# Performance work log

Measured on AMD Instinct MI355X. Metric: run time of the kernel, lower is better.

Reference implementation:

```python
import jax, jax.numpy as jnp
import numpy as np

EPS = 1e-5


def _cbr(z, W, bn, relu=True):
    # z: [b, Cin, L]; W: [Cout, Cin]; bn: [4, Cout] = (gamma, beta, mean, var)
    # 1x1 Conv2d (bias=False) over a [b, Cin, L, 1] tensor == channel matmul.
    y = jnp.einsum('oi,bil->bol', W, z)
    g, b_, m, v = bn[0], bn[1], bn[2], bn[3]
    y = g[:, None] * (y - m[:, None]) * jax.lax.rsqrt(v[:, None] + EPS) + b_[:, None]
    return jax.nn.relu(y) if relu else y


def setup_inputs() -> dict:
    key = jax.random.key(0)
    ks = jax.random.split(key, 13)
    b, c, h, w = 32, 512, 48, 48
    in_spatial = h * w          # 2304
    inter_spatial = in_spatial // 4  # 576
    inter_channel = c // 4      # 128
    ncc = 1 + inter_channel     # 129
    return {
        'x': jax.random.normal(ks[0], (b, c, h, w), jnp.float32),
        'W_theta': jax.random.normal(ks[1], (inter_spatial, in_spatial), jnp.float32) * 0.02,
        'bn_theta': jax.random.uniform(ks[2], (4, inter_spatial), jnp.float32),
        'W_phi': jax.random.normal(ks[3], (inter_spatial, in_spatial), jnp.float32) * 0.02,
        'bn_phi': jax.random.uniform(ks[4], (4, inter_spatial), jnp.float32),
        'W_gx': jax.random.normal(ks[5], (inter_spatial, in_spatial), jnp.float32) * 0.02,
        'bn_gx': jax.random.uniform(ks[6], (4, inter_spatial), jnp.float32),
        'W_gg': jax.random.normal(ks[7], (inter_channel, 2 * c), jnp.float32) * 0.02,
        'bn_gg': jax.random.uniform(ks[8], (4, inter_channel), jnp.float32),
        'W_c1': jax.random.normal(ks[9], (ncc // 2, ncc), jnp.float32) * 0.02,
        'bn_c1': jax.random.uniform(ks[10], (4, ncc // 2), jnp.float32),
        'W_c2': jax.random.normal(ks[11], (1, ncc // 2), jnp.float32) * 0.02,
        'bn_c2': jax.random.uniform(ks[12], (4, 1), jnp.float32),
    }


def reference(x, W_theta, bn_theta, W_phi, bn_phi, W_gx, bn_gx,
              W_gg, bn_gg, W_c1, bn_c1, W_c2, bn_c2):
    b, c, h, w = x.shape
    xc = x.reshape(b, c, h * w).transpose(0, 2, 1)          # [b, hw, c]
    xc1 = _cbr(xc, W_theta, bn_theta).transpose(0, 2, 1)    # [b, c, is]
    xc2 = _cbr(xc, W_phi, bn_phi)                           # [b, is, c]
    Gc = jnp.einsum('bcs,bsd->bcd', xc1, xc2)               # [b, c, c]
    Gc_joint = jnp.concatenate([Gc.transpose(0, 2, 1), Gc], axis=1)  # [b, 2c, c]
    Gc_joint = _cbr(Gc_joint, W_gg, bn_gg)                  # [b, ic, c]
    g_xc = _cbr(xc, W_gx, bn_gx).mean(axis=1, keepdims=True)  # [b, 1, c]
    yc = jnp.concatenate([g_xc, Gc_joint], axis=1)          # [b, 1+ic, c]
    wy = _cbr(yc, W_c1, bn_c1)
    wy = _cbr(wy, W_c2, bn_c2, relu=False)                  # [b, 1, c]
    gate = jax.nn.sigmoid(wy)[:, 0, :, None, None]          # [b, c, 1, 1]
    return gate * x + x
```

## Files before the change

### kernel.cpp

```cpp
#include <hip/hip_runtime.h>
#include <cstdint>

#define EPSV 1e-5f
typedef unsigned short u16;
typedef __attribute__((ext_vector_type(8))) short bh8;
typedef __attribute__((ext_vector_type(4))) float f4;

__device__ __forceinline__ float bf2f(u16 h) { return __uint_as_float((unsigned)h << 16); }
__device__ __forceinline__ u16 f2bf(float x) {
    unsigned u = __float_as_uint(x);
    u += 0x7fffu + ((u >> 16) & 1u);
    return (u16)(u >> 16);
}

__device__ __forceinline__ void gl16(const void* g, const void* s) {
    __builtin_amdgcn_global_load_lds(
        reinterpret_cast<const __attribute__((address_space(1))) void*>((uintptr_t)g),
        reinterpret_cast<__attribute__((address_space(3))) void*>((unsigned)(uintptr_t)s),
        16, 0, 0);
}

__device__ __forceinline__ void core2(
    const u16* __restrict__ Ah, const u16* __restrict__ Al,
    const u16* __restrict__ Bh, const u16* __restrict__ Bl,
    long ldA, long ldB, int K, int rowA0, int rowB0,
    u16* lds, f4 acc[4][4])
{
    const int tid = threadIdx.x, l = tid & 63, w = tid >> 6;
    const int wr = w >> 1, wc = w & 1;
    const int srow = tid >> 2;
    const int schunk = ((tid & 3) ^ ((tid >> 3) & 3)) << 3;
    const size_t aoff = (size_t)(rowA0 + srow) * ldA + schunk;
    const size_t boff = (size_t)(rowB0 + srow) * ldB + schunk;
    const size_t a64 = (size_t)64 * ldA, b64 = (size_t)64 * ldB;
    const int rr = l & 15, cq = l >> 4;
    const int roff = rr * 64 + (((cq ^ ((rr >> 1) & 3))) << 4);
    char* const base0 = (char*)lds;
    char* const base1 = (char*)lds + 32768;
    const int nt = K >> 5;

#define STAGE_SWZ(base, s0) do { \
    gl16(Ah + aoff + (s0),       (base) +         w * 1024); \
    gl16(Ah + aoff + a64 + (s0), (base) +  4096 + w * 1024); \
    gl16(Al + aoff + (s0),       (base) +  8192 + w * 1024); \
    gl16(Al + aoff + a64 + (s0), (base) + 12288 + w * 1024); \
    gl16(Bh + boff + (s0),       (base) + 16384 + w * 1024); \
    gl16(Bh + boff + b64 + (s0), (base) + 20480 + w * 1024); \
    gl16(Bl + boff + (s0),       (base) + 24576 + w * 1024); \
    gl16(Bl + boff + b64 + (s0), (base) + 28672 + w * 1024); \
} while (0)

    STAGE_SWZ(base0, 0);
    __syncthreads();
    int p = 0;
    for (int t = 0; t < nt; ++t) {
        if (t + 1 < nt) STAGE_SWZ(p ? base0 : base1, (size_t)(t + 1) << 5);
        const char* buf = p ? base1 : base0;
        bh8 a_h[4], a_l[4], b_h[4], b_l[4];
#pragma unroll
        for (int i = 0; i < 4; ++i) {
            a_h[i] = *(const bh8*)(buf + (wr * 4 + i) * 1024 + roff);
            a_l[i] = *(const bh8*)(buf + 8192 + (wr * 4 + i) * 1024 + roff);
            b_h[i] = *(const bh8*)(buf + 16384 + (wc * 4 + i) * 1024 + roff);
            b_l[i] = *(const bh8*)(buf + 24576 + (wc * 4 + i) * 1024 + roff);
        }
#pragma unroll
        for (int i = 0; i < 4; ++i)
#pragma unroll
            for (int j = 0; j < 4; ++j)
                acc[i][j] = __builtin_amdgcn_mfma_f32_16x16x32_bf16(a_h[i], b_h[j], acc[i][j], 0, 0, 0);
#pragma unroll
        for (int i = 0; i < 4; ++i)
#pragma unroll
            for (int j = 0; j < 4; ++j)
                acc[i][j] = __builtin_amdgcn_mfma_f32_16x16x32_bf16(a_h[i], b_l[j], acc[i][j], 0, 0, 0);
#pragma unroll
        for (int i = 0; i < 4; ++i)
#pragma unroll
            for (int j = 0; j < 4; ++j)
                acc[i][j] = __builtin_amdgcn_mfma_f32_16x16x32_bf16(a_l[i], b_h[j], acc[i][j], 0, 0, 0);
        __syncthreads();
        p ^= 1;
    }
#undef STAGE_SWZ
}

__global__ __launch_bounds__(256) void gemm_s1_v3(
    const u16* __restrict__ Xh, const u16* __restrict__ Xl,
    const u16* __restrict__ W0h, const u16* __restrict__ W0l,
    const u16* __restrict__ W1h, const u16* __restrict__ W1l,
    const u16* __restrict__ W2h, const u16* __restrict__ W2l,
    const float* __restrict__ bn0, const float* __restrict__ bn1,
    const float* __restrict__ bn2,
    u16* __restrict__ Y0h, u16* __restrict__ Y0l,
    u16* __restrict__ Y1h, u16* __restrict__ Y1l,
    u16* __restrict__ Y2h, u16* __restrict__ Y2l)
{
    const int h = blockIdx.x;
    const int orig = (h & 7) * 240 + (h >> 3);
    const int ow = orig % 15;
    const int rest = orig / 15;
    const int ct = rest & 3, bz = rest >> 2;
    const int wi = ow / 5, otw = ow % 5;

    const u16* Bh = wi == 0 ? W0h : wi == 1 ? W1h : W2h;
    const u16* Bl = wi == 0 ? W0l : wi == 1 ? W1l : W2l;
    const float* bnp = wi == 0 ? bn0 : wi == 1 ? bn1 : bn2;
    u16* Yh = wi == 0 ? Y0h : wi == 1 ? Y1h : Y2h;
    u16* Yl = wi == 0 ? Y0l : wi == 1 ? Y1l : Y2l;

    __shared__ u16 lds[32768];
    f4 acc[4][4];
    const f4 z4 = {0.f, 0.f, 0.f, 0.f};
#pragma unroll
    for (int i = 0; i < 4; ++i)
#pragma unroll
        for (int j = 0; j < 4; ++j) acc[i][j] = z4;

    core2(Xh, Xl, Bh, Bl, 2304, 2304, 2304,
          bz * 512 + ct * 128, otw * 128, lds, acc);

    const int l = threadIdx.x & 63, w = threadIdx.x >> 6;
    const int wr = w >> 1, wc = w & 1;
    const int mb = ct * 128 + wr * 64;
    const int nbw = otw * 128 + wc * 64;
    const int lm = l & 15;
#pragma unroll
    for (int j = 0; j < 4; ++j) {
        const int o = nbw + j * 16 + lm;
        const bool val = (o < 576);
        float sc = 0.f, sh = 0.f;
        if (val) {
            const float gg = bnp[o], be = bnp[576 + o], mm = bnp[1152 + o], vv = bnp[1728 + o];
            sc = gg * rsqrtf(vv + EPSV);
            sh = be - mm * sc;
        }
#pragma unroll
        for (int i = 0; i < 4; ++i) {
            const int c = mb + i * 16 + ((l >> 4) << 2);
#pragma unroll
            for (int r = 0; r < 4; ++r) {
                const float y = val ? fmaxf(acc[i][j][r] * sc + sh, 0.f) : 0.f;
                const u16 hh = f2bf(y);
                const u16 lo = f2bf(y - bf2f(hh));
                const size_t off = ((size_t)bz * 512 + c + r) * 640 + o;
                Yh[off] = hh; Yl[off] = lo;
            }
        }
    }
}

__global__ __launch_bounds__(256) void gemm_u(
    const u16* __restrict__ Wggh, const u16* __restrict__ Wggl,
    const u16* __restrict__ tnth, const u16* __restrict__ tntl,
    const u16* __restrict__ pnth, const u16* __restrict__ pntl,
    u16* __restrict__ U1h, u16* __restrict__ U1l,
    u16* __restrict__ U2h, u16* __restrict__ U2l)
{
    const int h = blockIdx.x;
    const int orig = (h & 7) * 40 + (h >> 3);
    const int ot = orig % 5;
    const int rest = orig / 5;
    const int u = rest & 1, b = rest >> 1;

    const u16* Ah = Wggh + (u ? 512 : 0);
    const u16* Al = Wggl + (u ? 512 : 0);
    const u16* Bh = u ? tnth : pnth;
    const u16* Bl = u ? tntl : pntl;

    __shared__ u16 lds[32768];
    f4 acc[4][4];
    const f4 z4 = {0.f, 0.f, 0.f, 0.f};
#pragma unroll
    for (int i = 0; i < 4; ++i)
#pragma unroll
        for (int j = 0; j < 4; ++j) acc[i][j] = z4;

    core2(Ah, Al, Bh, Bl, 1024, 512, 512, 0, b * 640 + ot * 128, lds, acc);

    u16* Uh = u ? U2h : U1h;
    u16* Ul = u ? U2l : U1l;
    const int l = threadIdx.x & 63, w = threadIdx.x >> 6;
    const int wr = w >> 1, wc = w & 1;
#pragma unroll
    for (int i = 0; i < 4; ++i)
#pragma unroll
        for (int j = 0; j < 4; ++j)
#pragma unroll
            for (int r = 0; r < 4; ++r) {
                const int irow = wr * 64 + i * 16 + ((l >> 4) << 2) + r;
                const int ocol = ot * 128 + wc * 64 + j * 16 + (l & 15);
                const float v = acc[i][j][r];
                const u16 hh = f2bf(v);
                const u16 lo = f2bf(v - bf2f(hh));
                const size_t off = ((size_t)b * 128 + irow) * 640 + ocol;
                Uh[off] = hh; Ul[off] = lo;
            }
}

__global__ __launch_bounds__(256) void gemm_term_p(
    const u16* __restrict__ U1h, const u16* __restrict__ U1l,
    const u16* __restrict__ U2h, const u16* __restrict__ U2l,
    const u16* __restrict__ tth, const u16* __restrict__ ttl,
    const u16* __restrict__ pth, const u16* __restrict__ ptl,
    float* __restrict__ GGa, float* __restrict__ GGb)
{
    const int h = blockIdx.x;
    const int orig = (h & 7) * 32 + (h >> 3);
    const int dt = orig & 3;
    const int u = (orig >> 2) & 1;
    const int b = orig >> 3;

    const u16* Ah = u ? U2h : U1h;
    const u16* Al = u ? U2l : U1l;
    const u16* Bh = u ? pth : tth;
    const u16* Bl = u ? ptl : ttl;
    float* G = u ? GGb : GGa;

    __shared__ u16 lds[32768];
    f4 acc[4][4];
    const f4 z4 = {0.f, 0.f, 0.f, 0.f};
#pragma unroll
    for (int i = 0; i < 4; ++i)
#pragma unroll
        for (int j = 0; j < 4; ++j) acc[i][j] = z4;

    core2(Ah, Al, Bh, Bl, 640, 640, 640,
          b * 128, b * 512 + dt * 128, lds, acc);

    const int l = threadIdx.x & 63, w = threadIdx.x >> 6;
    const int wr = w >> 1, wc = w & 1;
#pragma unroll
    for (int i = 0; i < 4; ++i)
#pragma unroll
        for (int j = 0; j < 4; ++j)
#pragma unroll
            for (int r = 0; r < 4; ++r) {
                const int irow = wr * 64 + i * 16 + ((l >> 4) << 2) + r;
                const int dcol = dt * 128 + wc * 64 + j * 16 + (l & 15);
                G[((size_t)b * 128 + irow) * 512 + dcol] = acc[i][j][r];
            }
}

__global__ __launch_bounds__(256) void gg_combine(
    float* __restrict__ GGa, const float* __restrict__ GGb,
    const float* __restrict__ bn, long n4)
{
    const long i = (long)blockIdx.x * 256 + threadIdx.x;
    if (i >= n4) return;
    const int irow = (int)((i >> 7) & 127);
    const float g = bn[irow], be = bn[128 + irow], m = bn[256 + irow], v = bn[384 + irow];
    const float sc = g * rsqrtf(v + EPSV);
    const float sh = be - m * sc;
    float4 a = ((const float4*)GGa)[i];
    const float4 b = ((const float4*)GGb)[i];
    a.x = fmaxf((a.x + b.x) * sc + sh, 0.f);
    a.y = fmaxf((a.y + b.y) * sc + sh, 0.f);
    a.z = fmaxf((a.z + b.z) * sc + sh, 0.f);
    a.w = fmaxf((a.w + b.w) * sc + sh, 0.f);
    ((float4*)GGa)[i] = a;
}

__global__ __launch_bounds__(256) void transpose_y(
    const u16* __restrict__ s0, u16* __restrict__ d0,
    const u16* __restrict__ s1, u16* __restrict__ d1,
    const u16* __restrict__ s2, u16* __restrict__ d2,
    const u16* __restrict__ s3, u16* __restrict__ d3)
{
    const int pz = blockIdx.z;
    const int b = pz >> 2, pl = pz & 3;
    const u16* src = pl == 0 ? s0 : pl == 1 ? s1 : pl == 2 ? s2 : s3;
    u16* dst = pl == 0 ? d0 : pl == 1 ? d1 : pl == 2 ? d2 : d3;
    const int o0 = blockIdx.x * 64, c0 = blockIdx.y * 64;
    __shared__ u16 t[64][72];
    const int tid = threadIdx.x;
#pragma unroll
    for (int rdx = tid; rdx < 512; rdx += 256) {
        const int c = rdx >> 3, oc = (rdx & 7) << 3;
        *(bh8*)&t[c][oc] = *(const bh8*)&src[((size_t)b * 512 + c0 + c) * 640 + o0 + oc];
    }
    __syncthreads();
#pragma unroll
    for (int wdx = tid; wdx < 512; wdx += 256) {
        const int o = wdx >> 3, cc = (wdx & 7) << 3;
        u16 v[8];
#pragma unroll
        for (int e = 0; e < 8; ++e) v[e] = t[cc + e][o];
        *(bh8*)&dst[((size_t)b * 640 + o0 + o) * 512 + c0 + cc] = *(bh8*)&v[0];
    }
}

__global__ __launch_bounds__(256) void conv_split(
    const float* __restrict__ in, u16* __restrict__ hi, u16* __restrict__ lo, long n8)
{
    long i = (long)blockIdx.x * 256 + threadIdx.x;
    const long stride = (long)gridDim.x * 256;
    for (; i < n8; i += stride) {
        const float4 a = ((const float4*)in)[2 * i];
        const float4 b = ((const float4*)in)[2 * i + 1];
        const float v[8] = {a.x, a.y, a.z, a.w, b.x, b.y, b.z, b.w};
        unsigned hw[4], lw[4];
#pragma unroll
        for (int k = 0; k < 4; ++k) {
            const u16 h0 = f2bf(v[2 * k]), h1 = f2bf(v[2 * k + 1]);
            const u16 l0 = f2bf(v[2 * k] - bf2f(h0)), l1 = f2bf(v[2 * k + 1] - bf2f(h1));
            hw[k] = (unsigned)h0 | ((unsigned)h1 << 16);
            lw[k] = (unsigned)l0 | ((unsigned)l1 << 16);
        }
        *(uint4*)&hi[8 * i] = make_uint4(hw[0], hw[1], hw[2], hw[3]);
        *(uint4*)&lo[8 * i] = make_uint4(lw[0], lw[1], lw[2], lw[3]);
    }
}

__global__ __launch_bounds__(256) void conv_w_pad(
    const float* __restrict__ W, u16* __restrict__ hi, u16* __restrict__ lo,
    int rows, long n8)
{
    const long i = (long)blockIdx.x * 256 + threadIdx.x;
    if (i >= n8) return;
    const long e = i * 8;
    const int row = (int)(e / 2304);
    unsigned hw[4] = {0, 0, 0, 0}, lw[4] = {0, 0, 0, 0};
    if (row < rows) {
        const float4 a = ((const float4*)W)[2 * i];
        const float4 b = ((const float4*)W)[2 * i + 1];
        const float v[8] = {a.x, a.y, a.z, a.w, b.x, b.y, b.z, b.w};
#pragma unroll
        for (int k = 0; k < 4; ++k) {
            const u16 h0 = f2bf(v[2 * k]), h1 = f2bf(v[2 * k + 1]);
            const u16 l0 = f2bf(v[2 * k] - bf2f(h0)), l1 = f2bf(v[2 * k + 1] - bf2f(h1));
            hw[k] = (unsigned)h0 | ((unsigned)h1 << 16);
            lw[k] = (unsigned)l0 | ((unsigned)l1 << 16);
        }
    }
    *(uint4*)&hi[8 * i] = make_uint4(hw[0], hw[1], hw[2], hw[3]);
    *(uint4*)&lo[8 * i] = make_uint4(lw[0], lw[1], lw[2], lw[3]);
}

__global__ __launch_bounds__(256) void row_mean(
    const u16* __restrict__ Yh, const u16* __restrict__ Yl,
    float* __restrict__ out, int rows)
{
    const int l = threadIdx.x & 63;
    const int row = blockIdx.x * 4 + (threadIdx.x >> 6);
    if (row >= rows) return;
    const u16* ph = Yh + (size_t)row * 640;
    const u16* pl = Yl + (size_t)row * 640;
    float s = 0.f;
    struct U8 { u16 u[8]; };
    for (int k = l; k < 80; k += 64) {
        const U8 a = *(const U8*)&ph[k * 8];
        const U8 b = *(const U8*)&pl[k * 8];
#pragma unroll
        for (int e = 0; e < 8; ++e) s += bf2f(a.u[e]) + bf2f(b.u[e]);
    }
    for (int off = 32; off; off >>= 1) s += __shfl_down(s, off, 64);
    if (l == 0) out[row] = s * (1.f / 576.f);
}

__global__ __launch_bounds__(256)
void gate_kernel(const float* __restrict__ gxc, const float* __restrict__ GG,
                 const float* __restrict__ Wc1, const float* __restrict__ bn1,
                 const float* __restrict__ Wc2, const float* __restrict__ bn2,
                 float* __restrict__ gate, int IC, int D, int OC)
{
    const int b  = blockIdx.y;
    const int d0 = blockIdx.x * 64;

    __shared__ float yc_s[129][64];
    __shared__ float part[4][64];

    const int tid = threadIdx.x;
    for (int idx = tid; idx < 129 * 64; idx += 256) {
        const int j = idx >> 6, d = idx & 63;
        yc_s[j][d] = (j == 0) ? gxc[b * D + d0 + d]
                              : GG[((size_t)b * IC + (j - 1)) * D + d0 + d];
    }
    __syncthreads();

    const int d = tid & 63;
    const int q = tid >> 6;
    float acc2 = 0.f;
    for (int o = q * 16; o < q * 16 + 16; ++o) {
        float s = 0.f;
        const float* __restrict__ w = &Wc1[o * 129];
        for (int j = 0; j < 129; ++j) s = fmaf(w[j], yc_s[j][d], s);
        const float g1 = bn1[o], be1 = bn1[OC + o], m1 = bn1[2 * OC + o], v1 = bn1[3 * OC + o];
        const float sc = g1 / sqrtf(v1 + EPSV);
        const float w1 = fmaxf(s * sc + (be1 - m1 * sc), 0.f);
        acc2 = fmaf(Wc2[o], w1, acc2);
    }
    part[q][d] = acc2;
    __syncthreads();
    if (q == 0) {
        const float s = part[0][d] + part[1][d] + part[2][d] + part[3][d];
        const float g2 = bn2[0], be2 = bn2[1], m2 = bn2[2], v2 = bn2[3];
        const float sc = g2 / sqrtf(v2 + EPSV);
        const float wy = s * sc + (be2 - m2 * sc);
        gate[b * D + d0 + d] = 1.f / (1.f + expf(-wy));
    }
}

__global__ __launch_bounds__(256)
void final_kernel(const float* __restrict__ x, const float* __restrict__ gate,
                  float* __restrict__ out, long n4, int sp4)
{
    long i = (long)blockIdx.x * blockDim.x + threadIdx.x;
    const long stride = (long)gridDim.x * blockDim.x;
    for (; i < n4; i += stride) {
        float4 v = ((const float4*)x)[i];
        const long bc = i / sp4;
        const float gm = 1.f + gate[bc];
        v.x *= gm; v.y *= gm; v.z *= gm; v.w *= gm;
        ((float4*)out)[i] = v;
    }
}

extern "C" void kernel_launch(void* const* d_in, const int* in_sizes, int n_in,
                              void* d_out, int out_size, void* d_ws, size_t ws_size,
                              hipStream_t stream)
{
    const float* x        = (const float*)d_in[0];
    const float* W_theta  = (const float*)d_in[1];
    const float* bn_theta = (const float*)d_in[2];
    const float* W_phi    = (const float*)d_in[3];
    const float* bn_phi   = (const float*)d_in[4];
    const float* W_gx     = (const float*)d_in[5];
    const float* bn_gx    = (const float*)d_in[6];
    const float* W_gg     = (const float*)d_in[7];
    const float* bn_gg    = (const float*)d_in[8];
    const float* W_c1     = (const float*)d_in[9];
    const float* bn_c1    = (const float*)d_in[10];
    const float* W_c2     = (const float*)d_in[11];
    const float* bn_c2    = (const float*)d_in[12];
    float* out = (float*)d_out;

    const int B = 32, C = 512, S = 2304, O = 576, OP = 640, IC = 128, OC = 64;
    const size_t P  = (size_t)B * C * OP;
    const size_t WP = (size_t)OP * S;
    const size_t UP = (size_t)B * IC * OP;

    u16* tth = (u16*)d_out;
    u16* ttl = tth + P;
    u16* pth = ttl + P;
    u16* ptl = pth + P;
    u16* Wgh = ptl + P;
    u16* Wgl = Wgh + WP;
    u16* Wth = Wgl + WP;
    u16* Wtl = Wth + WP;
    u16* Wph = Wtl + WP;
    u16* Wpl = Wph + WP;
    u16* wggh = Wpl + WP;
    u16* wggl = wggh + (size_t)IC * 1024;
    u16* u1h = wggl + (size_t)IC * 1024;
    u16* u1l = u1h + UP;
    u16* u2h = u1l + UP;
    u16* u2l = u2h + UP;
    float* GGa = (float*)(u2l + UP);
    float* GGb = GGa + (size_t)B * IC * C;

    u16* Xhi  = (u16*)d_ws;
    u16* Xlo  = Xhi + (size_t)B * C * S;
    u16* ygxh = Xlo + (size_t)B * C * S;
    u16* ygxl = ygxh + P;
    float* gxc  = (float*)(ygxl + P);
    float* gate = gxc + (size_t)B * C;
    u16* tnth = (u16*)d_ws;
    u16* tntl = tnth + P;
    u16* pnth = tntl + P;
    u16* pntl = pnth + P;

    const dim3 blk(256);

    const long wN8 = (long)WP / 8;
    conv_w_pad<<<dim3((unsigned)(wN8 / 256)), blk, 0, stream>>>(W_gx,    Wgh, Wgl, O, wN8);
    conv_w_pad<<<dim3((unsigned)(wN8 / 256)), blk, 0, stream>>>(W_theta, Wth, Wtl, O, wN8);
    conv_w_pad<<<dim3((unsigned)(wN8 / 256)), blk, 0, stream>>>(W_phi,   Wph, Wpl, O, wN8);
    conv_split<<<dim3(64), blk, 0, stream>>>(W_gg, wggh, wggl, (long)IC * 1024 / 8);

    conv_split<<<dim3(2048), blk, 0, stream>>>(x, Xhi, Xlo, (long)B * C * S / 8);
    gemm_s1_v3<<<dim3(1920), blk, 0, stream>>>(
        Xhi, Xlo, Wgh, Wgl, Wth, Wtl, Wph, Wpl,
        bn_gx, bn_theta, bn_phi,
        ygxh, ygxl, tth, ttl, pth, ptl);
    row_mean<<<dim3(4096), blk, 0, stream>>>(ygxh, ygxl, gxc, B * C);

    transpose_y<<<dim3(10, 8, 128), blk, 0, stream>>>(
        tth, tnth, ttl, tntl, pth, pnth, ptl, pntl);

    gemm_u<<<dim3(320), blk, 0, stream>>>(wggh, wggl, tnth, tntl, pnth, pntl,
                                          u1h, u1l, u2h, u2l);

    gemm_term_p<<<dim3(256), blk, 0, stream>>>(u1h, u1l, u2h, u2l,
                                               tth, ttl, pth, ptl, GGa, GGb);
    gg_combine<<<dim3(2048), blk, 0, stream>>>(GGa, GGb, bn_gg,
                                               (long)B * IC * C / 4);

    gate_kernel<<<dim3(C / 64, B), blk, 0, stream>>>(gxc, GGa, W_c1, bn_c1, W_c2, bn_c2,
                                                     gate, IC, C, OC);

    final_kernel<<<dim3(2048), blk, 0, stream>>>(x, gate, out,
                                                 (long)B * C * S / 4, S / 4);
}
```

Before: 682.8 us.

## Enlarge stage-1 GEMM tile to 256x128 and skip A-low term for g_x path

Replaces the 128x128 tile GEMM core with a 256x128 tile core (8x4 MFMA accumulators per wave, 96KB double-buffered LDS) and halves the grid to 960 blocks, which raises data reuse per loaded B tile. For the W_gx projection (wi==0) it also drops the A-low loads and the a_l*b_h MFMA pass, because that output is only averaged, so less precision is needed there. The cost is higher register pressure and larger LDS use, which lowers occupancy, plus slightly reduced accuracy on the g_x branch.

```diff
diff --git a/kernel.cpp b/kernel.cpp
--- a/kernel.cpp
+++ b/kernel.cpp
@@ -85,7 +85,85 @@
 #undef STAGE_SWZ
 }
 
-__global__ __launch_bounds__(256) void gemm_s1_v3(
+__device__ __forceinline__ void core3(
+    const u16* __restrict__ Ah, const u16* __restrict__ Al,
+    const u16* __restrict__ Bh, const u16* __restrict__ Bl,
+    long ldA, long ldB, int K, int rowA0, int rowB0, bool full,
+    u16* lds, f4 acc[8][4])
+{
+    const int tid = threadIdx.x, l = tid & 63, w = tid >> 6;
+    const int wr = w >> 1, wc = w & 1;
+    const int srow = tid >> 2;
+    const int schunk = ((tid & 3) ^ ((tid >> 3) & 3)) << 3;
+    const size_t aoff = (size_t)(rowA0 + srow) * ldA + schunk;
+    const size_t boff = (size_t)(rowB0 + srow) * ldB + schunk;
+    const size_t a64 = (size_t)64 * ldA, b64 = (size_t)64 * ldB;
+    const int rr = l & 15, cq = l >> 4;
+    const int roff = rr * 64 + (((cq ^ ((rr >> 1) & 3))) << 4);
+    char* const base0 = (char*)lds;
+    char* const base1 = (char*)lds + 49152;
+    const int nt = K >> 5;
+
+#define STAGE3(base, s0) do { \
+    gl16(Ah + aoff + (s0),           (base) +         w * 1024); \
+    gl16(Ah + aoff + a64 + (s0),     (base) +  4096 + w * 1024); \
+    gl16(Ah + aoff + 2*a64 + (s0),   (base) +  8192 + w * 1024); \
+    gl16(Ah + aoff + 3*a64 + (s0),   (base) + 12288 + w * 1024); \
+    if (full) { \
+        gl16(Al + aoff + (s0),         (base) + 16384 + w * 1024); \
+        gl16(Al + aoff + a64 + (s0),   (base) + 20480 + w * 1024); \
+        gl16(Al + aoff + 2*a64 + (s0), (base) + 24576 + w * 1024); \
+        gl16(Al + aoff + 3*a64 + (s0), (base) + 28672 + w * 1024); \
+    } \
+    gl16(Bh + boff + (s0),           (base) + 32768 + w * 1024); \
+    gl16(Bh + boff + b64 + (s0),     (base) + 36864 + w * 1024); \
+    gl16(Bl + boff + (s0),           (base) + 40960 + w * 1024); \
+    gl16(Bl + boff + b64 + (s0),     (base) + 45056 + w * 1024); \
+} while (0)
+
+    STAGE3(base0, 0);
+    __syncthreads();
+    int p = 0;
+    for (int t = 0; t < nt; ++t) {
+        if (t + 1 < nt) STAGE3(p ? base0 : base1, (size_t)(t + 1) << 5);
+        const char* buf = p ? base1 : base0;
+        bh8 a_h[8], b_h[4], b_l[4];
+#pragma unroll
+        for (int i = 0; i < 8; ++i)
+            a_h[i] = *(const bh8*)(buf + (wr * 8 + i) * 1024 + roff);
+#pragma unroll
+        for (int j = 0; j < 4; ++j) {
+            b_h[j] = *(const bh8*)(buf + 32768 + (wc * 4 + j) * 1024 + roff);
+            b_l[j] = *(const bh8*)(buf + 40960 + (wc * 4 + j) * 1024 + roff);
+        }
+#pragma unroll
+        for (int i = 0; i < 8; ++i)
+#pragma unroll
+            for (int j = 0; j < 4; ++j)
+                acc[i][j] = __builtin_amdgcn_mfma_f32_16x16x32_bf16(a_h[i], b_h[j], acc[i][j], 0, 0, 0);
+#pragma unroll
+        for (int i = 0; i < 8; ++i)
+#pragma unroll
+            for (int j = 0; j < 4; ++j)
+                acc[i][j] = __builtin_amdgcn_mfma_f32_16x16x32_bf16(a_h[i], b_l[j], acc[i][j], 0, 0, 0);
+        if (full) {
+            bh8 a_l[8];
+#pragma unroll
+            for (int i = 0; i < 8; ++i)
+                a_l[i] = *(const bh8*)(buf + 16384 + (wr * 8 + i) * 1024 + roff);
+#pragma unroll
+            for (int i = 0; i < 8; ++i)
+#pragma unroll
+                for (int j = 0; j < 4; ++j)
+                    acc[i][j] = __builtin_amdgcn_mfma_f32_16x16x32_bf16(a_l[i], b_h[j], acc[i][j], 0, 0, 0);
+        }
+        __syncthreads();
+        p ^= 1;
+    }
+#undef STAGE3
+}
+
+__global__ __launch_bounds__(256) void gemm_s1_v4(
     const u16* __restrict__ Xh, const u16* __restrict__ Xl,
     const u16* __restrict__ W0h, const u16* __restrict__ W0l,
     const u16* __restrict__ W1h, const u16* __restrict__ W1l,
@@ -97,11 +175,12 @@
     u16* __restrict__ Y2h, u16* __restrict__ Y2l)
 {
     const int h = blockIdx.x;
-    const int orig = (h & 7) * 240 + (h >> 3);
+    const int orig = (h & 7) * 120 + (h >> 3);
     const int ow = orig % 15;
     const int rest = orig / 15;
-    const int ct = rest & 3, bz = rest >> 2;
+    const int ct = rest & 1, bz = rest >> 1;
     const int wi = ow / 5, otw = ow % 5;
+    const bool full = (wi != 0);
 
     const u16* Bh = wi == 0 ? W0h : wi == 1 ? W1h : W2h;
     const u16* Bl = wi == 0 ? W0l : wi == 1 ? W1l : W2l;
@@ -109,20 +188,20 @@
     u16* Yh = wi == 0 ? Y0h : wi == 1 ? Y1h : Y2h;
     u16* Yl = wi == 0 ? Y0l : wi == 1 ? Y1l : Y2l;
 
-    __shared__ u16 lds[32768];
-    f4 acc[4][4];
+    __shared__ u16 lds[49152];
+    f4 acc[8][4];
     const f4 z4 = {0.f, 0.f, 0.f, 0.f};
 #pragma unroll
-    for (int i = 0; i < 4; ++i)
+    for (int i = 0; i < 8; ++i)
 #pragma unroll
         for (int j = 0; j < 4; ++j) acc[i][j] = z4;
 
-    core2(Xh, Xl, Bh, Bl, 2304, 2304, 2304,
-          bz * 512 + ct * 128, otw * 128, lds, acc);
+    core3(Xh, Xl, Bh, Bl, 2304, 2304, 2304,
+          bz * 512 + ct * 256, otw * 128, full, lds, acc);
 
     const int l = threadIdx.x & 63, w = threadIdx.x >> 6;
     const int wr = w >> 1, wc = w & 1;
-    const int mb = ct * 128 + wr * 64;
+    const int mb = ct * 256 + wr * 128;
     const int nbw = otw * 128 + wc * 64;
     const int lm = l & 15;
 #pragma unroll
@@ -136,7 +215,7 @@
             sh = be - mm * sc;
         }
 #pragma unroll
-        for (int i = 0; i < 4; ++i) {
+        for (int i = 0; i < 8; ++i) {
             const int c = mb + i * 16 + ((l >> 4) << 2);
 #pragma unroll
             for (int r = 0; r < 4; ++r) {
@@ -479,7 +558,7 @@
     conv_split<<<dim3(64), blk, 0, stream>>>(W_gg, wggh, wggl, (long)IC * 1024 / 8);
 
     conv_split<<<dim3(2048), blk, 0, stream>>>(x, Xhi, Xlo, (long)B * C * S / 8);
-    gemm_s1_v3<<<dim3(1920), blk, 0, stream>>>(
+    gemm_s1_v4<<<dim3(960), blk, 0, stream>>>(
         Xhi, Xlo, Wgh, Wgl, Wth, Wtl, Wph, Wpl,
         bn_gx, bn_theta, bn_phi,
         ygxh, ygxl, tth, ttl, pth, ptl);
```

New measurement: 680.6 us. No clear change (-0.3%).

## Rewrite stage-1 GEMM with 512-thread 256x128 tiles and triple-buffered pipeline

Applied to the files above, without the earlier changes.

Replaces the shared core2 mainloop in the stage-1 GEMM with an inlined kernel using 512 threads, a 256x128 output tile per block and a three-stage LDS ring buffer. Global-to-LDS loads are interleaved between MFMA phases using explicit vmcnt waits, barriers and setprio. It also drops the low-part A loads and the a_lo*b_hi MFMAs for the gx projection, which is only averaged afterwards. Intended to cut memory stalls and improve B-tile reuse, at the cost of larger LDS use (lower occupancy) and reduced precision for the gx branch.

```diff
diff --git a/kernel.cpp b/kernel.cpp
--- a/kernel.cpp
+++ b/kernel.cpp
@@ -85,7 +85,7 @@
 #undef STAGE_SWZ
 }
 
-__global__ __launch_bounds__(256) void gemm_s1_v3(
+__global__ __launch_bounds__(512) void gemm_s1_v6(
     const u16* __restrict__ Xh, const u16* __restrict__ Xl,
     const u16* __restrict__ W0h, const u16* __restrict__ W0l,
     const u16* __restrict__ W1h, const u16* __restrict__ W1l,
@@ -97,11 +97,12 @@
     u16* __restrict__ Y2h, u16* __restrict__ Y2l)
 {
     const int h = blockIdx.x;
-    const int orig = (h & 7) * 240 + (h >> 3);
+    const int orig = (h & 7) * 120 + (h >> 3);
     const int ow = orig % 15;
     const int rest = orig / 15;
-    const int ct = rest & 3, bz = rest >> 2;
+    const int ct = rest & 1, bz = rest >> 1;
     const int wi = ow / 5, otw = ow % 5;
+    const bool full = (wi != 0);
 
     const u16* Bh = wi == 0 ? W0h : wi == 1 ? W1h : W2h;
     const u16* Bl = wi == 0 ? W0l : wi == 1 ? W1l : W2l;
@@ -109,7 +110,32 @@
     u16* Yh = wi == 0 ? Y0h : wi == 1 ? Y1h : Y2h;
     u16* Yl = wi == 0 ? Y0l : wi == 1 ? Y1l : Y2l;
 
-    __shared__ u16 lds[32768];
+    __shared__ u16 lds[73728];
+
+    const int tid = threadIdx.x, l = tid & 63, w = tid >> 6;
+    const int wm = w >> 1, wn = w & 1;
+    const int srow = tid >> 2;
+    const int schunk = ((tid & 3) ^ ((tid >> 3) & 3)) << 3;
+    const long ldK = 2304;
+    const int rowA0 = bz * 512 + ct * 256;
+    const int rowB0 = otw * 128;
+    const size_t aoff = (size_t)(rowA0 + srow) * ldK + schunk;
+    const size_t boff = (size_t)(rowB0 + srow) * ldK + schunk;
+    const size_t a128 = (size_t)128 * ldK;
+    const int rr = l & 15, cq = l >> 4;
+    const int roff = rr * 64 + ((cq ^ ((rr >> 1) & 3)) << 4);
+    char* const ldsb = (char*)lds;
+    const int nt = 72;
+
+#define ST_AHI(sb, s0) do { \
+    gl16(Xh + aoff + (s0),        (sb) +         w * 1024); \
+    gl16(Xh + aoff + a128 + (s0), (sb) +  8192 + w * 1024); } while (0)
+#define ST_ALO(sb, s0) do { \
+    gl16(Xl + aoff + (s0),        (sb) + 16384 + w * 1024); \
+    gl16(Xl + aoff + a128 + (s0), (sb) + 24576 + w * 1024); } while (0)
+#define ST_BHI(sb, s0) gl16(Bh + boff + (s0), (sb) + 32768 + w * 1024)
+#define ST_BLO(sb, s0) gl16(Bl + boff + (s0), (sb) + 40960 + w * 1024)
+
     f4 acc[4][4];
     const f4 z4 = {0.f, 0.f, 0.f, 0.f};
 #pragma unroll
@@ -117,13 +143,84 @@
 #pragma unroll
         for (int j = 0; j < 4; ++j) acc[i][j] = z4;
 
-    core2(Xh, Xl, Bh, Bl, 2304, 2304, 2304,
-          bz * 512 + ct * 128, otw * 128, lds, acc);
-
-    const int l = threadIdx.x & 63, w = threadIdx.x >> 6;
-    const int wr = w >> 1, wc = w & 1;
-    const int mb = ct * 128 + wr * 64;
-    const int nbw = otw * 128 + wc * 64;
+    ST_AHI(ldsb, 0); if (full) ST_ALO(ldsb, 0); ST_BHI(ldsb, 0); ST_BLO(ldsb, 0);
+    ST_AHI(ldsb + 49152, 32); if (full) ST_ALO(ldsb + 49152, 32);
+    ST_BHI(ldsb + 49152, 32); ST_BLO(ldsb + 49152, 32);
+    if (full) asm volatile("s_waitcnt vmcnt(6)" ::: "memory");
+    else      asm volatile("s_waitcnt vmcnt(4)" ::: "memory");
+    __builtin_amdgcn_sched_barrier(0);
+    __builtin_amdgcn_s_barrier();
+
+    for (int t = 0; t < nt; ++t) {
+        const char* buf = ldsb + (t % 3) * 49152;
+        char* sbuf = ldsb + ((t + 2) % 3) * 49152;
+        const bool pre = (t + 2 < nt);
+        const int s0 = (t + 2) << 5;
+
+        bh8 a_h[4], b_h[4], a_l[4], b_l[4];
+#pragma unroll
+        for (int i = 0; i < 4; ++i)
+            a_h[i] = *(const bh8*)(buf + (wm * 4 + i) * 1024 + roff);
+#pragma unroll
+        for (int j = 0; j < 4; ++j)
+            b_h[j] = *(const bh8*)(buf + 32768 + (wn * 4 + j) * 1024 + roff);
+        if (pre) ST_AHI(sbuf, s0);
+        __builtin_amdgcn_s_barrier();
+        __builtin_amdgcn_s_setprio(1);
+#pragma unroll
+        for (int i = 0; i < 4; ++i)
+#pragma unroll
+            for (int j = 0; j < 4; ++j)
+                acc[i][j] = __builtin_amdgcn_mfma_f32_16x16x32_bf16(a_h[i], b_h[j], acc[i][j], 0, 0, 0);
+        __builtin_amdgcn_s_setprio(0);
+        __builtin_amdgcn_s_barrier();
+        if (full) {
+#pragma unroll
+            for (int i = 0; i < 4; ++i)
+                a_l[i] = *(const bh8*)(buf + 16384 + (wm * 4 + i) * 1024 + roff);
+        }
+#pragma unroll
+        for (int j = 0; j < 4; ++j)
+            b_l[j] = *(const bh8*)(buf + 40960 + (wn * 4 + j) * 1024 + roff);
+        if (pre) { if (full) ST_ALO(sbuf, s0); ST_BHI(sbuf, s0); }
+        __builtin_amdgcn_s_barrier();
+        __builtin_amdgcn_s_setprio(1);
+#pragma unroll
+        for (int i = 0; i < 4; ++i)
+#pragma unroll
+            for (int j = 0; j < 4; ++j)
+                acc[i][j] = __builtin_amdgcn_mfma_f32_16x16x32_bf16(a_h[i], b_l[j], acc[i][j], 0, 0, 0);
+        __builtin_amdgcn_s_setprio(0);
+        __builtin_amdgcn_s_barrier();
+        if (pre) ST_BLO(sbuf, s0);
+        if (t + 1 < nt) {
+            if (pre) {
+                if (full) asm volatile("s_waitcnt vmcnt(6)" ::: "memory");
+                else      asm volatile("s_waitcnt vmcnt(4)" ::: "memory");
+            } else {
+                asm volatile("s_waitcnt vmcnt(0)" ::: "memory");
+            }
+            __builtin_amdgcn_sched_barrier(0);
+        }
+        __builtin_amdgcn_s_barrier();
+        if (full) {
+            __builtin_amdgcn_s_setprio(1);
+#pragma unroll
+            for (int i = 0; i < 4; ++i)
+#pragma unroll
+                for (int j = 0; j < 4; ++j)
+                    acc[i][j] = __builtin_amdgcn_mfma_f32_16x16x32_bf16(a_l[i], b_h[j], acc[i][j], 0, 0, 0);
+            __builtin_amdgcn_s_setprio(0);
+        }
+        __builtin_amdgcn_s_barrier();
+    }
+#undef ST_AHI
+#undef ST_ALO
+#undef ST_BHI
+#undef ST_BLO
+
+    const int mb = ct * 256 + wm * 64;
+    const int nbw = otw * 128 + wn * 64;
     const int lm = l & 15;
 #pragma unroll
     for (int j = 0; j < 4; ++j) {
@@ -479,7 +576,7 @@
     conv_split<<<dim3(64), blk, 0, stream>>>(W_gg, wggh, wggl, (long)IC * 1024 / 8);
 
     conv_split<<<dim3(2048), blk, 0, stream>>>(x, Xhi, Xlo, (long)B * C * S / 8);
-    gemm_s1_v3<<<dim3(1920), blk, 0, stream>>>(
+    gemm_s1_v6<<<dim3(960), dim3(512), 0, stream>>>(
         Xhi, Xlo, Wgh, Wgl, Wth, Wtl, Wph, Wpl,
         bn_gx, bn_theta, bn_phi,
         ygxh, ygxl, tth, ttl, pth, ptl);
```

After: 633.2 us. 7.3% less time.
